# Kernel tuning notes

Hardware: AMD Instinct MI355X
Metric: run time of the kernel (lower is better)

Reference implementation:

```python
import jax, jax.numpy as jnp
import numpy as np

B, T, N, C = 4, 16, 50000, 16
E, DEG = 50000, 16
TOTAL = E * DEG
LAM = 0.3
COS_EPS = 1e-8   # torch cosine_similarity eps
NORM_EPS = 1e-8  # min-max normalization eps


def _build_window_dynamic_features(x_raw):
    # (B,T,N,C) -> (B,N,2C): per-node window mean and std as dynamic features
    mu = jnp.mean(x_raw, axis=1)
    sd = jnp.std(x_raw, axis=1)
    return jnp.concatenate([mu, sd], axis=-1)


def setup_inputs() -> dict:
    key = jax.random.key(0)
    k1, k2, k3, k4 = jax.random.split(key, 4)
    x_raw = jax.random.normal(k1, (B, T, N, C), dtype=jnp.float32)
    H = jnp.zeros((1, 1), dtype=jnp.float32)  # unused by forward; placeholder
    W = jax.random.uniform(k2, (E,), dtype=jnp.float32)
    edge_members = jax.random.randint(k3, (TOTAL,), 0, N, dtype=jnp.int32)
    edge_centers = jax.random.randint(k4, (E,), 0, N, dtype=jnp.int32)
    # CSR offsets, fixed degree DEG per hyperedge
    edge_offsets = jnp.arange(E + 1, dtype=jnp.int32) * DEG
    return {"x_raw": x_raw, "H": H, "W": W, "edge_members": edge_members,
            "edge_centers": edge_centers, "edge_offsets": edge_offsets}


def reference(x_raw, H, W, edge_members, edge_centers, edge_offsets):
    feat = _build_window_dynamic_features(x_raw)          # (B, N, D)
    E_ = W.shape[0]
    total = edge_members.shape[0]
    deg = edge_offsets[1:] - edge_offsets[:-1]            # (E,)
    member_edge_ids = jnp.repeat(jnp.arange(E_, dtype=jnp.int32), deg,
                                 total_repeat_length=total)  # (total,)

    member_feat = feat[:, edge_members, :]                       # (B, total, D)
    center_feat = feat[:, edge_centers[member_edge_ids], :]      # (B, total, D)

    # cosine similarity with torch-style eps clamping of norms
    dot = jnp.sum(member_feat * center_feat, axis=-1)            # (B, total)
    mn = jnp.maximum(jnp.linalg.norm(member_feat, axis=-1), COS_EPS)
    cn = jnp.maximum(jnp.linalg.norm(center_feat, axis=-1), COS_EPS)
    sim = jnp.clip(dot / (mn * cn), 0.0, 1.0)                    # (B, total)

    # segment scatter-add into per-edge bins, then mean
    sums = jax.ops.segment_sum(sim.T, member_edge_ids, num_segments=E_).T  # (B, E)
    counts = jnp.maximum(deg.astype(sim.dtype), 1.0)
    mean_sim = sums / counts[None, :]                            # (B, E)

    # per-batch min-max normalization
    smin = jnp.min(mean_sim, axis=1, keepdims=True)
    smax = jnp.max(mean_sim, axis=1, keepdims=True)
    mean_sim = (mean_sim - smin) / (smax - smin + NORM_EPS)

    return W[None, :] * (1.0 + LAM * mean_sim)                   # (B, E)
```

## Files before the change

### kernel.cpp

```cpp
#include <hip/hip_runtime.h>
#include <hip/hip_fp16.h>

#define Bn 4
#define Tn 16
#define Nn 50000
#define Cn 16
#define En 50000
#define LAM 0.3f
#define COS_EPS 1e-8f
#define NORM_EPS 1e-8f

union H8 { __half2 h2[4]; float4 f4; };

__global__ void feat_kernel(const float* __restrict__ x, float4* __restrict__ feat,
                            unsigned* __restrict__ mm) {
    if (blockIdx.x == 0 && threadIdx.x < 2 * Bn) {
        mm[threadIdx.x] = (threadIdx.x & 1) ? 0u : 0x7F800000u;
    }
    int gid = blockIdx.x * blockDim.x + threadIdx.x;
    if (gid >= Bn * Nn * 4) return;
    int c4 = gid & 3;
    int bn = gid >> 2;
    int b  = bn / Nn;
    int n  = bn - b * Nn;

    const float4* x4 = (const float4*)x;
    float4 s  = make_float4(0.f, 0.f, 0.f, 0.f);
    float4 ss = make_float4(0.f, 0.f, 0.f, 0.f);
    int base = (b * Tn) * Nn;
#pragma unroll
    for (int t = 0; t < Tn; ++t) {
        float4 v = x4[(base + t * Nn + n) * 4 + c4];
        s.x += v.x; s.y += v.y; s.z += v.z; s.w += v.w;
        ss.x += v.x * v.x; ss.y += v.y * v.y; ss.z += v.z * v.z; ss.w += v.w * v.w;
    }
    const float inv = 1.0f / (float)Tn;
    float4 m, sd;
    m.x = s.x * inv; m.y = s.y * inv; m.z = s.z * inv; m.w = s.w * inv;
    sd.x = sqrtf(fmaxf(ss.x * inv - m.x * m.x, 0.f));
    sd.y = sqrtf(fmaxf(ss.y * inv - m.y * m.y, 0.f));
    sd.z = sqrtf(fmaxf(ss.z * inv - m.z * m.z, 0.f));
    sd.w = sqrtf(fmaxf(ss.w * inv - m.w * m.w, 0.f));

    float p = m.x * m.x + m.y * m.y + m.z * m.z + m.w * m.w
            + sd.x * sd.x + sd.y * sd.y + sd.z * sd.z + sd.w * sd.w;
    p += __shfl_xor(p, 1);
    p += __shfl_xor(p, 2);
    float rn = 1.0f / fmaxf(sqrtf(p), COS_EPS);

    H8 o;
    o.h2[0] = __floats2half2_rn(m.x * rn,  m.y * rn);
    o.h2[1] = __floats2half2_rn(m.z * rn,  m.w * rn);
    o.h2[2] = __floats2half2_rn(sd.x * rn, sd.y * rn);
    o.h2[3] = __floats2half2_rn(sd.z * rn, sd.w * rn);
    feat[(n * 4 + b) * 4 + c4] = o.f4;
}

__global__ void edge_sim_kernel(const float4* __restrict__ feat,
                                const int* __restrict__ members,
                                const int* __restrict__ centers,
                                const int* __restrict__ offsets,
                                float* __restrict__ ms) {
    int tid  = blockIdx.x * blockDim.x + threadIdx.x;
    int e    = tid >> 6;
    if (e >= En) return;
    int lane = threadIdx.x & 63;
    int g    = lane >> 2;
    int q    = lane & 3;

    int off0 = offsets[e];
    int off1 = offsets[e + 1];
    int deg  = off1 - off0;
    int cn   = centers[e];

    float cf[Bn][8];
#pragma unroll
    for (int b_ = 0; b_ < Bn; ++b_) {
        H8 u; u.f4 = feat[(cn * 4 + b_) * 4 + q];
#pragma unroll
        for (int i = 0; i < 4; ++i) {
            float2 p = __half22float2(u.h2[i]);
            cf[b_][2 * i]     = p.x;
            cf[b_][2 * i + 1] = p.y;
        }
    }

    float sums[Bn] = {0.f, 0.f, 0.f, 0.f};
    for (int m0 = g; m0 < deg; m0 += 16) {
        int mn = members[off0 + m0];
#pragma unroll
        for (int b_ = 0; b_ < Bn; ++b_) {
            H8 u; u.f4 = feat[(mn * 4 + b_) * 4 + q];
            float d = 0.f;
#pragma unroll
            for (int i = 0; i < 4; ++i) {
                float2 p = __half22float2(u.h2[i]);
                d += p.x * cf[b_][2 * i] + p.y * cf[b_][2 * i + 1];
            }
            d += __shfl_xor(d, 1);
            d += __shfl_xor(d, 2);
            sums[b_] += fminf(fmaxf(d, 0.f), 1.f);
        }
    }
#pragma unroll
    for (int b_ = 0; b_ < Bn; ++b_) {
        float s = sums[b_];
        s += __shfl_xor(s, 4);
        s += __shfl_xor(s, 8);
        s += __shfl_xor(s, 16);
        s += __shfl_xor(s, 32);
        sums[b_] = s;
    }
    if (lane == 0) {
        float invd = 1.0f / fmaxf((float)deg, 1.0f);
#pragma unroll
        for (int b_ = 0; b_ < Bn; ++b_) ms[b_ * En + e] = sums[b_] * invd;
    }
}

__global__ void minmax_kernel(const float* __restrict__ ms, unsigned* __restrict__ mm) {
    int b = blockIdx.x >> 6;
    int j = blockIdx.x & 63;
    const float* p = ms + b * En;
    float lo = INFINITY, hi = 0.f;
    for (int i = j * blockDim.x + threadIdx.x; i < En; i += 64 * 256) {
        float v = p[i];
        lo = fminf(lo, v);
        hi = fmaxf(hi, v);
    }
#pragma unroll
    for (int m = 1; m < 64; m <<= 1) {
        lo = fminf(lo, __shfl_xor(lo, m));
        hi = fmaxf(hi, __shfl_xor(hi, m));
    }
    __shared__ float slo[4], shi[4];
    int wid  = threadIdx.x >> 6;
    int lane = threadIdx.x & 63;
    if (lane == 0) { slo[wid] = lo; shi[wid] = hi; }
    __syncthreads();
    if (threadIdx.x == 0) {
        float flo = fminf(fminf(slo[0], slo[1]), fminf(slo[2], slo[3]));
        float fhi = fmaxf(fmaxf(shi[0], shi[1]), fmaxf(shi[2], shi[3]));
        atomicMin(&mm[b * 2],     __float_as_uint(flo));
        atomicMax(&mm[b * 2 + 1], __float_as_uint(fhi));
    }
}

__global__ void out_kernel(const float* __restrict__ ms, const unsigned* __restrict__ mm,
                           const float* __restrict__ W, float* __restrict__ out) {
    int gid = blockIdx.x * blockDim.x + threadIdx.x;
    if (gid >= Bn * En) return;
    int b = gid / En;
    int e = gid - b * En;
    float smin = __uint_as_float(mm[b * 2]);
    float smax = __uint_as_float(mm[b * 2 + 1]);
    float v = (ms[gid] - smin) / (smax - smin + NORM_EPS);
    out[gid] = W[e] * (1.0f + LAM * v);
}

extern "C" void kernel_launch(void* const* d_in, const int* in_sizes, int n_in,
                              void* d_out, int out_size, void* d_ws, size_t ws_size,
                              hipStream_t stream) {
    const float* x_raw        = (const float*)d_in[0];
    const float* W            = (const float*)d_in[2];
    const int*   edge_members = (const int*)d_in[3];
    const int*   edge_centers = (const int*)d_in[4];
    const int*   edge_offsets = (const int*)d_in[5];
    float*       out          = (float*)d_out;

    float4*   feat = (float4*)d_ws;
    float*    ms   = (float*)((char*)d_ws + (size_t)Nn * Bn * 64);
    unsigned* mm   = (unsigned*)(ms + (size_t)Bn * En);

    {
        int total = Bn * Nn * 4;
        feat_kernel<<<(total + 255) / 256, 256, 0, stream>>>(x_raw, feat, mm);
    }
    {
        long long threads = (long long)En * 64;
        int blocks = (int)((threads + 255) / 256);
        edge_sim_kernel<<<blocks, 256, 0, stream>>>(
            feat, edge_members, edge_centers, edge_offsets, ms);
    }
    minmax_kernel<<<Bn * 64, 256, 0, stream>>>(ms, mm);
    {
        int total = Bn * En;
        out_kernel<<<(total + 255) / 256, 256, 0, stream>>>(ms, mm, W, out);
    }
}
```

Measured before the change: 77.55 us.

## Split feature table per batch and launch edge similarity with batch grid dimension

Feature layout changes from node-major interleaved batches to batch-major slabs, and the edge similarity kernel gets a second grid dimension over batch so each wave handles one batch. Each batch's gather working set becomes a contiguous slab of about 3.2 MB that may fit better in cache, instead of 12.8 MB of interleaved data. In exchange, member indices, offsets and center loads are read four times, and four times as many waves are launched, each doing less work.

After: 105.7 us. 36.3% more time.

```diff
diff --git a/kernel.cpp b/kernel.cpp
--- a/kernel.cpp
+++ b/kernel.cpp
@@ -53,7 +53,7 @@
     o.h2[1] = __floats2half2_rn(m.z * rn,  m.w * rn);
     o.h2[2] = __floats2half2_rn(sd.x * rn, sd.y * rn);
     o.h2[3] = __floats2half2_rn(sd.z * rn, sd.w * rn);
-    feat[(n * 4 + b) * 4 + c4] = o.f4;
+    feat[(size_t)bn * 4 + c4] = o.f4;
 }
 
 __global__ void edge_sim_kernel(const float4* __restrict__ feat,
@@ -64,6 +64,7 @@
     int tid  = blockIdx.x * blockDim.x + threadIdx.x;
     int e    = tid >> 6;
     if (e >= En) return;
+    int b    = blockIdx.y;
     int lane = threadIdx.x & 63;
     int g    = lane >> 2;
     int q    = lane & 3;
@@ -73,49 +74,39 @@
     int deg  = off1 - off0;
     int cn   = centers[e];
 
-    float cf[Bn][8];
-#pragma unroll
-    for (int b_ = 0; b_ < Bn; ++b_) {
-        H8 u; u.f4 = feat[(cn * 4 + b_) * 4 + q];
+    const float4* slab = feat + (size_t)b * Nn * 4;
+
+    float cf[8];
+    {
+        H8 u; u.f4 = slab[cn * 4 + q];
 #pragma unroll
         for (int i = 0; i < 4; ++i) {
             float2 p = __half22float2(u.h2[i]);
-            cf[b_][2 * i]     = p.x;
-            cf[b_][2 * i + 1] = p.y;
+            cf[2 * i]     = p.x;
+            cf[2 * i + 1] = p.y;
         }
     }
 
-    float sums[Bn] = {0.f, 0.f, 0.f, 0.f};
+    float ssum = 0.f;
     for (int m0 = g; m0 < deg; m0 += 16) {
         int mn = members[off0 + m0];
+        H8 u; u.f4 = slab[mn * 4 + q];
+        float d = 0.f;
 #pragma unroll
-        for (int b_ = 0; b_ < Bn; ++b_) {
-            H8 u; u.f4 = feat[(mn * 4 + b_) * 4 + q];
-            float d = 0.f;
-#pragma unroll
-            for (int i = 0; i < 4; ++i) {
-                float2 p = __half22float2(u.h2[i]);
-                d += p.x * cf[b_][2 * i] + p.y * cf[b_][2 * i + 1];
-            }
-            d += __shfl_xor(d, 1);
-            d += __shfl_xor(d, 2);
-            sums[b_] += fminf(fmaxf(d, 0.f), 1.f);
+        for (int i = 0; i < 4; ++i) {
+            float2 p = __half22float2(u.h2[i]);
+            d += p.x * cf[2 * i] + p.y * cf[2 * i + 1];
         }
+        d += __shfl_xor(d, 1);
+        d += __shfl_xor(d, 2);
+        ssum += fminf(fmaxf(d, 0.f), 1.f);
     }
-#pragma unroll
-    for (int b_ = 0; b_ < Bn; ++b_) {
-        float s = sums[b_];
-        s += __shfl_xor(s, 4);
-        s += __shfl_xor(s, 8);
-        s += __shfl_xor(s, 16);
-        s += __shfl_xor(s, 32);
-        sums[b_] = s;
-    }
-    if (lane == 0) {
-        float invd = 1.0f / fmaxf((float)deg, 1.0f);
-#pragma unroll
-        for (int b_ = 0; b_ < Bn; ++b_) ms[b_ * En + e] = sums[b_] * invd;
-    }
+    ssum += __shfl_xor(ssum, 4);
+    ssum += __shfl_xor(ssum, 8);
+    ssum += __shfl_xor(ssum, 16);
+    ssum += __shfl_xor(ssum, 32);
+
+    if (lane == 0) ms[b * En + e] = ssum / fmaxf((float)deg, 1.0f);
 }
 
 __global__ void minmax_kernel(const float* __restrict__ ms, unsigned* __restrict__ mm) {
@@ -169,7 +160,7 @@
     float*       out          = (float*)d_out;
 
     float4*   feat = (float4*)d_ws;
-    float*    ms   = (float*)((char*)d_ws + (size_t)Nn * Bn * 64);
+    float*    ms   = (float*)((char*)d_ws + (size_t)Bn * Nn * 64);
     unsigned* mm   = (unsigned*)(ms + (size_t)Bn * En);
 
     {
@@ -177,9 +168,8 @@
         feat_kernel<<<(total + 255) / 256, 256, 0, stream>>>(x_raw, feat, mm);
     }
     {
-        long long threads = (long long)En * 64;
-        int blocks = (int)((threads + 255) / 256);
-        edge_sim_kernel<<<blocks, 256, 0, stream>>>(
+        dim3 grid((unsigned)(((long long)En * 64 + 255) / 256), Bn);
+        edge_sim_kernel<<<grid, 256, 0, stream>>>(
             feat, edge_members, edge_centers, edge_offsets, ms);
     }
     minmax_kernel<<<Bn * 64, 256, 0, stream>>>(ms, mm);
```
